# Performance work log

Measured on AMD Instinct MI355X. Metric: run time of the kernel, lower is better.

Reference implementation:

```python
import jax, jax.numpy as jnp
import numpy as np

NBITS = 4
OUT_F = 2048
IN_F = 2048


def _bit_ste(w, nbits):
    # clamp to [-1,1], quantize magnitude to nbits levels, keep sign
    step = float(2 ** nbits - 1)
    w = jnp.clip(w, -1.0, 1.0)
    return jnp.round(jnp.abs(w) * step) / step * jnp.sign(w)


def setup_inputs() -> dict:
    key = jax.random.key(0)
    ks = jax.random.split(key, 6)
    ex = np.arange(NBITS - 1, -1, -1)
    exps = jnp.asarray(2.0 ** ex / (2.0 ** NBITS - 1), dtype=jnp.float32)
    inp = {
        "input": jax.random.normal(ks[0], (8, 2048, IN_F), dtype=jnp.float32),
        # bit-plane weights: sigmoid of these gives soft bits in (0,1)
        "pweight": jax.random.normal(ks[1], (OUT_F, IN_F, NBITS), dtype=jnp.float32),
        "nweight": jax.random.normal(ks[2], (OUT_F, IN_F, NBITS), dtype=jnp.float32),
        "exps": exps,
        "bexps": exps,
        "mask_weight": jnp.ones((NBITS,), dtype=jnp.float32),  # init.constant_(1)
        "scale": jnp.array([0.05], dtype=jnp.float32),
        "pbias": jax.random.uniform(ks[3], (OUT_F, NBITS), dtype=jnp.float32, minval=0.0, maxval=float(2 ** NBITS - 1)) // 1.0 % 2.0,
        "nbias": jax.random.uniform(ks[4], (OUT_F, NBITS), dtype=jnp.float32, minval=0.0, maxval=float(2 ** NBITS - 1)) // 1.0 % 2.0,
        "biasscale": jnp.array([0.05], dtype=jnp.float32),
    }
    return inp


def reference(input, pweight, nweight, exps, bexps, mask_weight, scale, pbias, nbias, biasscale):
    temp = 1.0
    # temp_s and mask_discrete are all-ones buffers -> identity factors
    mask = jax.nn.sigmoid(mask_weight)                      # [N]
    soft = jax.nn.sigmoid(temp * pweight) - jax.nn.sigmoid(temp * nweight)  # [O,I,N]
    weight = jnp.einsum('oin,n->oi', soft, exps * mask) * scale[0]          # [O,I]
    bias_raw = jnp.einsum('on,n->o', pbias - nbias, bexps)  # [O]
    bias = _bit_ste(bias_raw, NBITS) * biasscale[0]
    # F.linear: y = x @ W^T + b
    return jnp.einsum('bsi,oi->bso', input, weight) + bias
```

## Files before the change

kernel.cpp:

```cpp
#include <hip/hip_runtime.h>
#include <hip/hip_bf16.h>
#include <stdint.h>

#define M_DIM 16384
#define N_DIM 2048
#define K_DIM 2048

typedef __attribute__((ext_vector_type(8))) __bf16 bf16x8;
typedef __attribute__((ext_vector_type(4))) float f32x4;

__device__ __forceinline__ unsigned short f2bf(float f) {
  unsigned int u = __builtin_bit_cast(unsigned int, f);
  u += 0x7FFFu + ((u >> 16) & 1u);
  return (unsigned short)(u >> 16);
}

__device__ __forceinline__ float sigmoidf_(float x) {
  return 1.0f / (1.0f + __expf(-x));
}

__global__ __launch_bounds__(256) void convert_x(const float4* __restrict__ x,
                                                 uint4* __restrict__ xb) {
  int idx = blockIdx.x * 256 + threadIdx.x;
  float4 a = x[idx * 2];
  float4 b = x[idx * 2 + 1];
  uint4 r;
  r.x = (unsigned)f2bf(a.x) | ((unsigned)f2bf(a.y) << 16);
  r.y = (unsigned)f2bf(a.z) | ((unsigned)f2bf(a.w) << 16);
  r.z = (unsigned)f2bf(b.x) | ((unsigned)f2bf(b.y) << 16);
  r.w = (unsigned)f2bf(b.z) | ((unsigned)f2bf(b.w) << 16);
  xb[idx] = r;
}

__global__ __launch_bounds__(256) void make_w(const float4* __restrict__ pw,
                                              const float4* __restrict__ nw,
                                              const float* __restrict__ exps,
                                              const float* __restrict__ maskw,
                                              const float* __restrict__ scale,
                                              unsigned short* __restrict__ wout) {
  int idx = blockIdx.x * 256 + threadIdx.x;
  float4 p = pw[idx];
  float4 n = nw[idx];
  float s = scale[0];
  float c0 = sigmoidf_(maskw[0]) * exps[0] * s;
  float c1 = sigmoidf_(maskw[1]) * exps[1] * s;
  float c2 = sigmoidf_(maskw[2]) * exps[2] * s;
  float c3 = sigmoidf_(maskw[3]) * exps[3] * s;
  float w = (sigmoidf_(p.x) - sigmoidf_(n.x)) * c0
          + (sigmoidf_(p.y) - sigmoidf_(n.y)) * c1
          + (sigmoidf_(p.z) - sigmoidf_(n.z)) * c2
          + (sigmoidf_(p.w) - sigmoidf_(n.w)) * c3;
  wout[idx] = f2bf(w);
}

__global__ __launch_bounds__(256) void make_bias(const float* __restrict__ pb,
                                                 const float* __restrict__ nb,
                                                 const float* __restrict__ bexps,
                                                 const float* __restrict__ bscale,
                                                 float* __restrict__ bias) {
  int o = blockIdx.x * 256 + threadIdx.x;
  if (o < N_DIM) {
    float x = 0.f;
#pragma unroll
    for (int n = 0; n < 4; ++n) x += (pb[o * 4 + n] - nb[o * 4 + n]) * bexps[n];
    float xc = fminf(fmaxf(x, -1.f), 1.f);
    float mag = rintf(fabsf(xc) * 15.f) * (1.f / 15.f);
    float sgn = (xc > 0.f) ? 1.f : ((xc < 0.f) ? -1.f : 0.f);
    bias[o] = mag * sgn * bscale[0];
  }
}


#define BM 256
#define BN 256
#define BK 64
#define NT (K_DIM / BK)

__device__ __forceinline__ void gload16(const void* g, void* l) {
  __builtin_amdgcn_global_load_lds(
      (const __attribute__((address_space(1))) unsigned int*)g,
      (__attribute__((address_space(3))) unsigned int*)l, 16, 0, 0);
}

#define VMCNT(n) asm volatile("s_waitcnt vmcnt(" #n ")" ::: "memory")
#define BAR() __builtin_amdgcn_s_barrier()

__global__ __launch_bounds__(512, 2) void gemm_bias(const unsigned short* __restrict__ X,
                                                    const unsigned short* __restrict__ W,
                                                    const float* __restrict__ bias,
                                                    float* __restrict__ out) {
  __shared__ unsigned short sA[2][BM * BK];
  __shared__ unsigned short sB[2][BN * BK];

  const int tid = threadIdx.x;
  const int swz = ((int)blockIdx.x & 7) * 64 + ((int)blockIdx.x >> 3);
  const int bm = swz >> 3;
  const int bn = swz & 7;
  const int row0 = bm * BM, col0 = bn * BN;

  const int w = tid >> 6, l = tid & 63;
  const int wr = w >> 2;
  const int wc = w & 3;
  const int lr = l & 15;
  const int lk4 = l >> 4;
  const int l7 = l & 7;

  const unsigned short* Ag = X + (size_t)row0 * K_DIM;
  const unsigned short* Bg = W + (size_t)col0 * K_DIM;

  const int srl = (tid >> 3) & 31;
  const int sc16 = (tid & 7) ^ ((tid >> 3) & 7);
  const int shi = tid >> 8;
  const int slin = ((tid >> 3) & 24) * 64 + (tid & 63) * 8;

  auto stage = [&](unsigned short* lbase, const unsigned short* gbase,
                   int rb0, int rb1, int tk) {
    int rb = shi ? rb1 : rb0;
    int trow = rb + srl;
    gload16(gbase + (size_t)trow * K_DIM + tk * BK + sc16 * 8,
            lbase + rb * 64 + slin);
  };

  auto rdA = [&](const unsigned short* base, int mf, int ks) -> bf16x8 {
    int trow = wr * 128 + mf * 16 + lr;
    int c16l = (ks * 4 + lk4) ^ l7;
    return *(const bf16x8*)&base[trow * 64 + c16l * 8];
  };
  auto rdB = [&](const unsigned short* base, int nf, int ks) -> bf16x8 {
    int trow = wc * 64 + nf * 16 + lr;
    int c16l = (ks * 4 + lk4) ^ l7;
    return *(const bf16x8*)&base[trow * 64 + c16l * 8];
  };

  f32x4 acc[8][4] = {};
  bf16x8 a[4][2], b[4][2];

#define PHASE_MFMA(mh, nh)                                                    \
  __builtin_amdgcn_s_setprio(1);                                              \
  _Pragma("unroll") for (int i = 0; i < 4; ++i)                               \
  _Pragma("unroll") for (int j = 0; j < 2; ++j)                               \
  _Pragma("unroll") for (int ks = 0; ks < 2; ++ks)                            \
      acc[(mh) * 4 + i][(nh) * 2 + j] = __builtin_amdgcn_mfma_f32_16x16x32_bf16( \
          a[i][ks], b[(nh) * 2 + j][ks], acc[(mh) * 4 + i][(nh) * 2 + j], 0, 0, 0); \
  __builtin_amdgcn_s_setprio(0);

  stage(sA[0], Ag, 0, 32, 0);
  stage(sA[0], Ag, 128, 160, 0);
  stage(sB[0], Bg, 0, 64, 0);
  stage(sB[0], Bg, 128, 192, 0);
  stage(sB[0], Bg, 32, 96, 0);
  stage(sB[0], Bg, 160, 224, 0);
  stage(sA[0], Ag, 64, 96, 0);
  stage(sA[0], Ag, 192, 224, 0);
  stage(sA[1], Ag, 0, 32, 1);
  stage(sA[1], Ag, 128, 160, 1);
  stage(sB[1], Bg, 0, 64, 1);
  stage(sB[1], Bg, 128, 192, 1);
  VMCNT(8);
  BAR();

  for (int t = 0; t < NT; ++t) {
    const int p = t & 1, q = p ^ 1;
    const int t1 = (t + 1) & (NT - 1);
    const int t2 = (t + 2) & (NT - 1);
    const unsigned short* pa = sA[p];
    const unsigned short* pb = sB[p];

#pragma unroll
    for (int i = 0; i < 4; ++i)
#pragma unroll
      for (int ks = 0; ks < 2; ++ks) a[i][ks] = rdA(pa, i, ks);
#pragma unroll
    for (int j = 0; j < 2; ++j)
#pragma unroll
      for (int ks = 0; ks < 2; ++ks) b[j][ks] = rdB(pb, j, ks);
    stage(sB[q], Bg, 32, 96, t1);
    stage(sB[q], Bg, 160, 224, t1);
    stage(sA[q], Ag, 64, 96, t1);
    stage(sA[q], Ag, 192, 224, t1);
    BAR();
    PHASE_MFMA(0, 0);
    VMCNT(10);
    BAR();

#pragma unroll
    for (int j = 2; j < 4; ++j)
#pragma unroll
      for (int ks = 0; ks < 2; ++ks) b[j][ks] = rdB(pb, j, ks);
    BAR();
    PHASE_MFMA(0, 1);
    VMCNT(8);
    BAR();

#pragma unroll
    for (int i = 0; i < 4; ++i)
#pragma unroll
      for (int ks = 0; ks < 2; ++ks) a[i][ks] = rdA(pa, 4 + i, ks);
    BAR();
    PHASE_MFMA(1, 0);
    BAR();

    stage(sA[p], Ag, 0, 32, t2);
    stage(sA[p], Ag, 128, 160, t2);
    stage(sB[p], Bg, 0, 64, t2);
    stage(sB[p], Bg, 128, 192, t2);
    BAR();
    PHASE_MFMA(1, 1);
    VMCNT(8);
    BAR();
  }

  float bv[4];
#pragma unroll
  for (int nf = 0; nf < 4; ++nf) bv[nf] = bias[col0 + wc * 64 + nf * 16 + lr];
  const int orow = lk4 * 4;
#pragma unroll
  for (int mf = 0; mf < 8; ++mf) {
#pragma unroll
    for (int nf = 0; nf < 4; ++nf) {
      const int colg = col0 + wc * 64 + nf * 16 + lr;
#pragma unroll
      for (int r = 0; r < 4; ++r) {
        int rowg = row0 + wr * 128 + mf * 16 + orow + r;
        out[(size_t)rowg * N_DIM + colg] = acc[mf][nf][r] + bv[nf];
      }
    }
  }
#undef PHASE_MFMA
}

extern "C" void kernel_launch(void* const* d_in, const int* in_sizes, int n_in,
                              void* d_out, int out_size, void* d_ws, size_t ws_size,
                              hipStream_t stream) {
  const float* input  = (const float*)d_in[0];
  const float* pweight = (const float*)d_in[1];
  const float* nweight = (const float*)d_in[2];
  const float* exps   = (const float*)d_in[3];
  const float* bexps  = (const float*)d_in[4];
  const float* maskw  = (const float*)d_in[5];
  const float* scale  = (const float*)d_in[6];
  const float* pbias  = (const float*)d_in[7];
  const float* nbias  = (const float*)d_in[8];
  const float* bscale = (const float*)d_in[9];
  float* out = (float*)d_out;

  unsigned short* Xb = (unsigned short*)d_ws;
  unsigned short* Wb = (unsigned short*)((char*)d_ws + (size_t)M_DIM * K_DIM * 2);
  float* bias = (float*)((char*)d_ws + (size_t)M_DIM * K_DIM * 2 + (size_t)N_DIM * K_DIM * 2);

  convert_x<<<(M_DIM * (size_t)K_DIM) / 8 / 256, 256, 0, stream>>>((const float4*)input, (uint4*)Xb);
  make_w<<<((size_t)N_DIM * K_DIM) / 256, 256, 0, stream>>>(
      (const float4*)pweight, (const float4*)nweight, exps, maskw, scale, Wb);
  make_bias<<<(N_DIM + 255) / 256, 256, 0, stream>>>(pbias, nbias, bexps, bscale, bias);

  dim3 grid((M_DIM / BM) * (N_DIM / BN));
  gemm_bias<<<grid, 512, 0, stream>>>(Xb, Wb, bias, out);
}
```

Before: 223.0 us.

## Software-pipeline LDS fragment reads across MFMA phases with double-buffered A registers

Restructures the main GEMM loop so each phase's LDS fragment reads for the next phase are issued alongside that phase's MFMAs, using two A register sets and prefetching the next tile's first fragments from the other LDS buffer. This removes the separate barrier between LDS reads and MFMA in each phase, cutting barriers from eight to four per iteration, and hides LDS latency behind matrix math. In exchange it uses more VGPRs and changes the vmcnt wait points, which adds occupancy and correctness-of-sync risk.

```diff
diff --git a/kernel.cpp b/kernel.cpp
--- a/kernel.cpp
+++ b/kernel.cpp
@@ -133,15 +133,17 @@
   };
 
   f32x4 acc[8][4] = {};
-  bf16x8 a[4][2], b[4][2];
-
-#define PHASE_MFMA(mh, nh)                                                    \
+  bf16x8 a0[4][2];
+  bf16x8 a1[4][2];
+  bf16x8 bb[4][2];
+
+#define PHASE_MFMA(AARR, MB, JB)                                              \
   __builtin_amdgcn_s_setprio(1);                                              \
   _Pragma("unroll") for (int i = 0; i < 4; ++i)                               \
-  _Pragma("unroll") for (int j = 0; j < 2; ++j)                               \
+  _Pragma("unroll") for (int jj = 0; jj < 2; ++jj)                            \
   _Pragma("unroll") for (int ks = 0; ks < 2; ++ks)                            \
-      acc[(mh) * 4 + i][(nh) * 2 + j] = __builtin_amdgcn_mfma_f32_16x16x32_bf16( \
-          a[i][ks], b[(nh) * 2 + j][ks], acc[(mh) * 4 + i][(nh) * 2 + j], 0, 0, 0); \
+      acc[(MB) + i][(JB) + jj] = __builtin_amdgcn_mfma_f32_16x16x32_bf16(     \
+          AARR[i][ks], bb[(JB) + jj][ks], acc[(MB) + i][(JB) + jj], 0, 0, 0); \
   __builtin_amdgcn_s_setprio(0);
 
   stage(sA[0], Ag, 0, 32, 0);
@@ -158,6 +160,16 @@
   stage(sB[1], Bg, 128, 192, 1);
   VMCNT(8);
   BAR();
+#pragma unroll
+  for (int i = 0; i < 4; ++i)
+#pragma unroll
+    for (int ks = 0; ks < 2; ++ks) a0[i][ks] = rdA(sA[0], i, ks);
+#pragma unroll
+  for (int j = 0; j < 2; ++j)
+#pragma unroll
+    for (int ks = 0; ks < 2; ++ks) bb[j][ks] = rdB(sB[0], j, ks);
+  VMCNT(6);
+  BAR();
 
   for (int t = 0; t < NT; ++t) {
     const int p = t & 1, q = p ^ 1;
@@ -165,48 +177,47 @@
     const int t2 = (t + 2) & (NT - 1);
     const unsigned short* pa = sA[p];
     const unsigned short* pb = sB[p];
-
-#pragma unroll
-    for (int i = 0; i < 4; ++i)
-#pragma unroll
-      for (int ks = 0; ks < 2; ++ks) a[i][ks] = rdA(pa, i, ks);
-#pragma unroll
-    for (int j = 0; j < 2; ++j)
-#pragma unroll
-      for (int ks = 0; ks < 2; ++ks) b[j][ks] = rdB(pb, j, ks);
+    const unsigned short* qa = sA[q];
+    const unsigned short* qb = sB[q];
+
+#pragma unroll
+    for (int j = 2; j < 4; ++j)
+#pragma unroll
+      for (int ks = 0; ks < 2; ++ks) bb[j][ks] = rdB(pb, j, ks);
     stage(sB[q], Bg, 32, 96, t1);
     stage(sB[q], Bg, 160, 224, t1);
+    PHASE_MFMA(a0, 0, 0);
+    VMCNT(6);
+    BAR();
+
+#pragma unroll
+    for (int i = 0; i < 4; ++i)
+#pragma unroll
+      for (int ks = 0; ks < 2; ++ks) a1[i][ks] = rdA(pa, 4 + i, ks);
     stage(sA[q], Ag, 64, 96, t1);
     stage(sA[q], Ag, 192, 224, t1);
-    BAR();
-    PHASE_MFMA(0, 0);
-    VMCNT(10);
-    BAR();
-
-#pragma unroll
-    for (int j = 2; j < 4; ++j)
-#pragma unroll
-      for (int ks = 0; ks < 2; ++ks) b[j][ks] = rdB(pb, j, ks);
-    BAR();
-    PHASE_MFMA(0, 1);
-    VMCNT(8);
+    PHASE_MFMA(a0, 0, 2);
+    VMCNT(6);
     BAR();
 
 #pragma unroll
     for (int i = 0; i < 4; ++i)
 #pragma unroll
-      for (int ks = 0; ks < 2; ++ks) a[i][ks] = rdA(pa, 4 + i, ks);
-    BAR();
-    PHASE_MFMA(1, 0);
-    BAR();
-
+      for (int ks = 0; ks < 2; ++ks) a0[i][ks] = rdA(qa, i, ks);
     stage(sA[p], Ag, 0, 32, t2);
     stage(sA[p], Ag, 128, 160, t2);
+    PHASE_MFMA(a1, 4, 0);
+    VMCNT(6);
+    BAR();
+
+#pragma unroll
+    for (int j = 0; j < 2; ++j)
+#pragma unroll
+      for (int ks = 0; ks < 2; ++ks) bb[j][ks] = rdB(qb, j, ks);
     stage(sB[p], Bg, 0, 64, t2);
     stage(sB[p], Bg, 128, 192, t2);
-    BAR();
-    PHASE_MFMA(1, 1);
-    VMCNT(8);
+    PHASE_MFMA(a1, 4, 2);
+    VMCNT(6);
     BAR();
   }
 
```

New measurement: 211.9 us. -5.0%, faster.
